# Performance work log

Hardware: AMD Instinct MI355X
Metric: run time of the kernel (lower is better)

## Reference

```python
import jax, jax.numpy as jnp
import numpy as np

B, T, C, H = 4, 1024, 512, 4
D = C // H
N_LAYER, LAYER_ID = 12, 1


def setup_inputs() -> dict:
    key = jax.random.key(0)
    ks = jax.random.split(key, 10)
    w = lambda k, shape: 0.02 * jax.random.normal(k, shape, dtype=jnp.float32)

    r01 = LAYER_ID / (N_LAYER - 1)          # ratio_0_to_1
    r1a0 = 1.0 - LAYER_ID / N_LAYER          # ratio_1_to_almost0
    i = np.arange(C, dtype=np.float32)
    time_decay = (-5.0 + 8.0 * (i / (C - 1)) ** (0.7 + 1.3 * r01)).astype(np.float32)
    xv = i / C
    tm_q = (xv ** r1a0).astype(np.float32)[None, None, :]
    tm_k = (xv ** r1a0).astype(np.float32)[None, None, :]
    tm_v = ((xv ** r1a0) + 0.3 * r01).astype(np.float32)[None, None, :]
    tm_g = (xv ** (0.5 * r1a0)).astype(np.float32)[None, None, :]

    return dict(
        x=jax.random.normal(ks[0], (B, T, C), dtype=jnp.float32),
        ln1_g=jnp.ones((C,), jnp.float32), ln1_b=jnp.zeros((C,), jnp.float32),
        ln2_g=jnp.ones((C,), jnp.float32), ln2_b=jnp.zeros((C,), jnp.float32),
        time_decay=jnp.asarray(time_decay),
        tm_q=jnp.asarray(tm_q), tm_k=jnp.asarray(tm_k),
        tm_v=jnp.asarray(tm_v), tm_g=jnp.asarray(tm_g),
        Wq=w(ks[1], (C, C)), Wk=w(ks[2], (C, C)), Wv=w(ks[3], (C, C)),
        Wg=w(ks[4], (C, C)), Wo=w(ks[5], (C, C)),
        rms_scale=jnp.ones((C,), jnp.float32),
        W1=w(ks[6], (4 * C, C)), W2=w(ks[7], (C, 4 * C)),
    )


def layernorm(x, g, b, eps=1e-5):
    m = x.mean(-1, keepdims=True)
    v = ((x - m) ** 2).mean(-1, keepdims=True)
    return g * (x - m) / jnp.sqrt(v + eps) + b


def rmsnorm(x, scale, eps=1e-8):
    # matches: norm = ||x||_2 / sqrt(dim); out = scale * x / (norm + eps)
    norm = jnp.sqrt(jnp.sum(x * x, axis=-1, keepdims=True)) / (x.shape[-1] ** 0.5)
    return scale * (x / (norm + eps))


def lnssm_scan(q, k, v, lam):
    """Decayed linear-attention scan. q,k,v: [B,T,H,D]; lam: [H,D] (decay over k index).
    Returns S: [B,T,H,D] = q_t^T A_t, Zs: [B,T,H] = q_t . z_t."""
    qT, kT, vT = (jnp.moveaxis(a, 1, 0) for a in (q, k, v))  # [T,B,H,D]
    Bq = q.shape[0]
    A0 = jnp.zeros((Bq, q.shape[2], q.shape[3], q.shape[3]), q.dtype)
    z0 = jnp.zeros((Bq, q.shape[2], q.shape[3]), q.dtype)

    def step(carry, inp):
        A, z = carry
        qt, kt, vt = inp
        A = lam[None, :, :, None] * A + kt[..., None] * vt[..., None, :]  # [B,H,Dk,Dv]
        z = lam[None] * z + kt                                            # [B,H,Dk]
        St = jnp.einsum('bhi,bhij->bhj', qt, A)
        Zt = jnp.einsum('bhi,bhi->bh', qt, z)
        return (A, z), (St, Zt)

    _, (S, Zs) = jax.lax.scan(step, (A0, z0), (qT, kT, vT))
    return jnp.moveaxis(S, 0, 1), jnp.moveaxis(Zs, 0, 1)


def reference(x, ln1_g, ln1_b, ln2_g, ln2_b, time_decay, tm_q, tm_k, tm_v, tm_g,
              Wq, Wk, Wv, Wg, Wo, rms_scale, W1, W2):
    Bx, Tx, Cx = x.shape
    Hh, Dd = H, Cx // H

    # --- TimeMix on ln1(x) ---
    h = layernorm(x, ln1_g, ln1_b)
    xx = jnp.concatenate([jnp.zeros_like(h[:, :1]), h[:, :-1]], axis=1)  # time shift
    xq = h * tm_q + xx * (1 - tm_q)
    xk = h * tm_k + xx * (1 - tm_k)
    xv_ = h * tm_v + xx * (1 - tm_v)
    xg = h * tm_g + xx * (1 - tm_g)
    q = xq @ Wq.T
    k = xk @ Wk.T
    v = xv_ @ Wv.T
    g = jax.nn.sigmoid(xg @ Wg.T)
    q = jnp.exp(rmsnorm(q, rms_scale))
    k = jnp.exp(rmsnorm(k, rms_scale))

    lam = jnp.exp(-jnp.exp(time_decay)).reshape(Hh, Dd)
    qh = q.reshape(Bx, Tx, Hh, Dd)
    kh = k.reshape(Bx, Tx, Hh, Dd)
    vh = v.reshape(Bx, Tx, Hh, Dd)
    S, Zs = lnssm_scan(qh, kh, vh, lam)
    att = (S / Zs[..., None]).reshape(Bx, Tx, Cx)
    att = (g * att) @ Wo.T
    x = x + att

    # --- ChannelMix on ln2(x) ---
    h2 = layernorm(x, ln2_g, ln2_b)
    x = x + jax.nn.gelu(h2 @ W1.T, approximate=False) @ W2.T
    return x
```

## Files before the change

### kernel.cpp

```cpp
#include <hip/hip_runtime.h>
#include <math.h>

#define Bb 4
#define Tt 1024
#define Cc 512
#define Hh 4
#define Dd 128
#define Mrows (Bb*Tt)
#define NC 32
#define CL 32
#define AUGSZ (Dd*(Dd+1))
#define AUGSTRIDE (16*AUGSZ)
#define AUGB_CB 18432

typedef unsigned short u16;
typedef __attribute__((ext_vector_type(8))) short bf16x8;
typedef __attribute__((ext_vector_type(4))) float f32x4;

__device__ __forceinline__ float readlane_f(float v, int lane) {
  return __uint_as_float(__builtin_amdgcn_readlane(__float_as_uint(v), lane));
}
__device__ __forceinline__ u16 f2bf(float f) {
  unsigned u = __float_as_uint(f);
  unsigned r = (u + 0x7fffu + ((u >> 16) & 1u)) >> 16;
  return (u16)r;
}
__device__ __forceinline__ unsigned pack2(float a, float b) {
  return (unsigned)f2bf(a) | ((unsigned)f2bf(b) << 16);
}

__global__ __launch_bounds__(256) void ln_kernel(const float* __restrict__ x,
    const float* __restrict__ g, const float* __restrict__ bta, float* __restrict__ out)
{
  int row = blockIdx.x, tid = threadIdx.x;
  const float* xr = x + (size_t)row * Cc;
  float v0 = xr[tid], v1 = xr[tid + 256];
  float s = v0 + v1, s2 = v0*v0 + v1*v1;
  #pragma unroll
  for (int off = 32; off > 0; off >>= 1) {
    s  += __shfl_down(s,  off, 64);
    s2 += __shfl_down(s2, off, 64);
  }
  __shared__ float rs[4], rq[4];
  int w = tid >> 6;
  if ((tid & 63) == 0) { rs[w] = s; rq[w] = s2; }
  __syncthreads();
  float S  = rs[0]+rs[1]+rs[2]+rs[3];
  float S2 = rq[0]+rq[1]+rq[2]+rq[3];
  float mean = S * (1.0f/Cc);
  float var  = S2 * (1.0f/Cc) - mean*mean;
  float inv = rsqrtf(var + 1e-5f);
  out[(size_t)row*Cc + tid]       = g[tid]     * (v0-mean)*inv + bta[tid];
  out[(size_t)row*Cc + tid + 256] = g[tid+256] * (v1-mean)*inv + bta[tid+256];
}

__global__ __launch_bounds__(256) void ln2b_kernel(const float* __restrict__ x,
    const float* __restrict__ p0, const float* __restrict__ p1,
    const float* __restrict__ g, const float* __restrict__ bta,
    float* __restrict__ x1, u16* __restrict__ out)
{
  int row = blockIdx.x, tid = threadIdx.x;
  size_t r0 = (size_t)row * Cc + tid, r1 = r0 + 256;
  float v0 = x[r0] + p0[r0] + p1[r0];
  float v1 = x[r1] + p0[r1] + p1[r1];
  x1[r0] = v0; x1[r1] = v1;
  float s = v0 + v1, s2 = v0*v0 + v1*v1;
  #pragma unroll
  for (int off = 32; off > 0; off >>= 1) {
    s  += __shfl_down(s,  off, 64);
    s2 += __shfl_down(s2, off, 64);
  }
  __shared__ float rs[4], rq[4];
  int w = tid >> 6;
  if ((tid & 63) == 0) { rs[w] = s; rq[w] = s2; }
  __syncthreads();
  float S  = rs[0]+rs[1]+rs[2]+rs[3];
  float S2 = rq[0]+rq[1]+rq[2]+rq[3];
  float mean = S * (1.0f/Cc);
  float var  = S2 * (1.0f/Cc) - mean*mean;
  float inv = rsqrtf(var + 1e-5f);
  int c0 = tid, c1 = tid + 256;
  float o0 = g[c0] * (v0-mean)*inv + bta[c0];
  float o1 = g[c1] * (v1-mean)*inv + bta[c1];
  out[((size_t)(c0 >> 3) * Mrows + row) * 8 + (c0 & 7)] = f2bf(o0);
  out[((size_t)(c1 >> 3) * Mrows + row) * 8 + (c1 & 7)] = f2bf(o1);
}

__device__ __forceinline__ void mix_one(const float* tm, int c0,
    float4 ha, float4 hb, float4 xa, float4 xb, u16* dst, size_t i8)
{
  float4 ta = *(const float4*)(tm + c0);
  float4 tb = *(const float4*)(tm + c0 + 4);
  uint4 o;
  o.x = pack2(ha.x*ta.x + xa.x*(1.f-ta.x), ha.y*ta.y + xa.y*(1.f-ta.y));
  o.y = pack2(ha.z*ta.z + xa.z*(1.f-ta.z), ha.w*ta.w + xa.w*(1.f-ta.w));
  o.z = pack2(hb.x*tb.x + xb.x*(1.f-tb.x), hb.y*tb.y + xb.y*(1.f-tb.y));
  o.w = pack2(hb.z*tb.z + xb.z*(1.f-tb.z), hb.w*tb.w + xb.w*(1.f-tb.w));
  *(uint4*)(dst + i8) = o;
}

__global__ __launch_bounds__(256) void mix_kernel(const float* __restrict__ h,
    const float* __restrict__ tmq, const float* __restrict__ tmk,
    const float* __restrict__ tmv, const float* __restrict__ tmg,
    u16* __restrict__ xqb, u16* __restrict__ xkb,
    u16* __restrict__ xvb, u16* __restrict__ xgb)
{
  int i = blockIdx.x * 256 + threadIdx.x;
  int m = i & 4095, c0 = (i >> 12) << 3;
  const float* hp = h + (size_t)m*Cc + c0;
  float4 ha = *(const float4*)hp, hb = *(const float4*)(hp + 4);
  float4 xa = make_float4(0,0,0,0), xb = make_float4(0,0,0,0);
  if (m & 1023) { xa = *(const float4*)(hp - Cc); xb = *(const float4*)(hp - Cc + 4); }
  size_t i8 = (size_t)i * 8;
  mix_one(tmq, c0, ha, hb, xa, xb, xqb, i8);
  mix_one(tmk, c0, ha, hb, xa, xb, xkb, i8);
  mix_one(tmv, c0, ha, hb, xa, xb, xvb, i8);
  mix_one(tmg, c0, ha, hb, xa, xb, xgb, i8);
}

__global__ __launch_bounds__(256) void wconv_all_kernel(
    const float* __restrict__ Wq, const float* __restrict__ Wk,
    const float* __restrict__ Wv, const float* __restrict__ Wg,
    const float* __restrict__ Wo, const float* __restrict__ W1,
    const float* __restrict__ W2, u16* __restrict__ out)
{
  int blk = blockIdx.x;
  const float* src; u16* dst; int K, nshift;
  if (blk < 640) {
    int wsel = blk >> 7;
    src = wsel==0?Wq:wsel==1?Wk:wsel==2?Wv:wsel==3?Wg:Wo;
    dst = out + (size_t)wsel*262144; K = 512; nshift = 9; blk &= 127;
  } else if (blk < 1152) {
    src = W1; dst = out + (size_t)5*262144; K = 512; nshift = 11; blk -= 640;
  } else {
    src = W2; dst = out + (size_t)5*262144 + 1048576; K = 2048; nshift = 9; blk -= 1152;
  }
  int i = blk*256 + threadIdx.x;
  int n = i & ((1 << nshift) - 1), kg = i >> nshift;
  const float* p = src + (size_t)n * K + kg * 8;
  float4 a = *(const float4*)p, b = *(const float4*)(p + 4);
  uint4 o;
  o.x = pack2(a.x, a.y); o.y = pack2(a.z, a.w);
  o.z = pack2(b.x, b.y); o.w = pack2(b.z, b.w);
  *(uint4*)(dst + (size_t)i * 8) = o;
}

template<int MR, int NR, int KR>
__device__ __forceinline__ void gemm_core(const u16* __restrict__ A,
    const u16* __restrict__ W, const float* __restrict__ res,
    float* __restrict__ outf, u16* __restrict__ outb, int act,
    int m0, int n0, u16* Asm, u16* Bsm)
{
  const int tid = threadIdx.x, w = tid >> 6, l = tid & 63;
  const int wr = w >> 1, wc = w & 1;
  f32x4 acc[4][4];
  #pragma unroll
  for (int i = 0; i < 4; ++i)
    #pragma unroll
    for (int j = 0; j < 4; ++j) acc[i][j] = (f32x4){0.f,0.f,0.f,0.f};
  const int kgl = l >> 4, rl = l & 15;
  const int q = w * 4;

  #define STAGE(KT, BUF) do {                                               \
    _Pragma("unroll")                                                       \
    for (int ii = 0; ii < 4; ++ii) {                                        \
      int qq = q + ii;                                                      \
      int isB = qq >> 3, idx = qq & 7, kg = idx >> 1, hf = idx & 1;         \
      const u16* src = isB                                                  \
        ? W + ((size_t)((KT)*4 + kg) * NR + n0 + hf*64 + l) * 8             \
        : A + ((size_t)((KT)*4 + kg) * MR + m0 + hf*64 + l) * 8;            \
      u16* dst = (isB ? Bsm : Asm) + (BUF)*4096 + (kg * 128 + hf * 64) * 8; \
      __builtin_amdgcn_global_load_lds(                                     \
          (const __attribute__((address_space(1))) void*)src,               \
          (__attribute__((address_space(3))) void*)dst, 16, 0, 0);          \
    }                                                                       \
  } while (0)

  constexpr int nk = KR >> 5;
  STAGE(0, 0); STAGE(1, 1);
  int cur = 0;
  for (int kt = 0; kt < nk; ++kt) {
    if (kt == nk - 1) asm volatile("s_waitcnt vmcnt(0)" ::: "memory");
    else              asm volatile("s_waitcnt vmcnt(4)" ::: "memory");
    __builtin_amdgcn_s_barrier();
    bf16x8 af[4], bfr[4];
    #pragma unroll
    for (int f = 0; f < 4; ++f)
      af[f] = *(const bf16x8*)&Asm[cur*4096 + (kgl*128 + wr*64 + f*16 + rl) * 8];
    #pragma unroll
    for (int f = 0; f < 4; ++f)
      bfr[f] = *(const bf16x8*)&Bsm[cur*4096 + (kgl*128 + wc*64 + f*16 + rl) * 8];
    if (kt + 2 < nk) {
      int nb = cur + 2; if (nb >= 3) nb -= 3;
      STAGE(kt + 2, nb);
    }
    __builtin_amdgcn_s_setprio(1);
    #pragma unroll
    for (int i = 0; i < 4; ++i)
      #pragma unroll
      for (int j = 0; j < 4; ++j)
        acc[i][j] = __builtin_amdgcn_mfma_f32_16x16x32_bf16(af[i], bfr[j], acc[i][j], 0, 0, 0);
    __builtin_amdgcn_s_setprio(0);
    if (++cur == 3) cur = 0;
  }
  #undef STAGE

  const int rbase = (l >> 4) * 4, cn = l & 15;
  #pragma unroll
  for (int i = 0; i < 4; ++i) {
    #pragma unroll
    for (int j = 0; j < 4; ++j) {
      #pragma unroll
      for (int r = 0; r < 4; ++r) {
        int m = m0 + wr*64 + i*16 + rbase + r;
        int n = n0 + wc*64 + j*16 + cn;
        float vv = acc[i][j][r];
        if (res) vv += res[(size_t)m * NR + n];
        if (act == 1) vv = 0.5f*vv*(1.f + erff(vv * 0.70710678118f));
        else if (act == 2) vv = 1.f/(1.f + expf(-vv));
        if (outb) outb[((size_t)(n >> 3) * MR + m) * 8 + (n & 7)] = f2bf(vv);
        else outf[(size_t)m * NR + n] = vv;
      }
    }
  }
}

__global__ __launch_bounds__(256) void gemm_qkvg(const u16* __restrict__ xall,
    const u16* __restrict__ Wall, float* __restrict__ outall)
{
  __shared__ __align__(16) u16 Asm[3*4096];
  __shared__ __align__(16) u16 Bsm[3*4096];
  int z = blockIdx.z;
  const size_t E = (size_t)Mrows * Cc;
  gemm_core<Mrows,512,512>(xall + z*E, Wall + (size_t)z*262144, nullptr,
            outall + z*E, nullptr, z == 3 ? 2 : 0,
            blockIdx.y * 128, blockIdx.x * 128, Asm, Bsm);
}

__global__ __launch_bounds__(256) void gemm_wo(const u16* __restrict__ A,
    const u16* __restrict__ W, float* __restrict__ pbuf)
{
  __shared__ __align__(16) u16 Asm[3*4096];
  __shared__ __align__(16) u16 Bsm[3*4096];
  int z = blockIdx.z;
  const size_t E = (size_t)Mrows * Cc;
  gemm_core<Mrows,512,256>(A + (size_t)z*32*Mrows*8, W + (size_t)z*32*512*8, nullptr,
            pbuf + z*E, nullptr, 0, blockIdx.y * 128, blockIdx.x * 128, Asm, Bsm);
}

__global__ __launch_bounds__(256) void gemm_w1(const u16* __restrict__ A,
    const u16* __restrict__ W, u16* __restrict__ outb)
{
  __shared__ __align__(16) u16 Asm[3*4096];
  __shared__ __align__(16) u16 Bsm[3*4096];
  gemm_core<Mrows,2048,512>(A, W, nullptr, nullptr, outb, 1,
            blockIdx.y * 128, blockIdx.x * 128, Asm, Bsm);
}

__global__ __launch_bounds__(256) void gemm_w2(const u16* __restrict__ A,
    const u16* __restrict__ W, float* __restrict__ pbuf)
{
  __shared__ __align__(16) u16 Asm[3*4096];
  __shared__ __align__(16) u16 Bsm[3*4096];
  int z = blockIdx.z;
  const size_t E = (size_t)Mrows * Cc;
  gemm_core<Mrows,512,512>(A + (size_t)z*64*Mrows*8, W + (size_t)z*64*512*8, nullptr,
            pbuf + z*E, nullptr, 0, blockIdx.y * 128, blockIdx.x * 128, Asm, Bsm);
}

__global__ __launch_bounds__(256) void reduce4_kernel(const float* __restrict__ x1,
    const float* __restrict__ p, float* __restrict__ out)
{
  const size_t E = (size_t)Mrows * Cc;
  size_t f = ((size_t)blockIdx.x * 256 + threadIdx.x) * 4;
  float4 a = *(const float4*)(x1 + f);
  float4 q0 = *(const float4*)(p + f);
  float4 q1 = *(const float4*)(p + E + f);
  float4 q2 = *(const float4*)(p + 2*E + f);
  float4 q3 = *(const float4*)(p + 3*E + f);
  float4 o;
  o.x = a.x + q0.x + q1.x + q2.x + q3.x;
  o.y = a.y + q0.y + q1.y + q2.y + q3.y;
  o.z = a.z + q0.z + q1.z + q2.z + q3.z;
  o.w = a.w + q0.w + q1.w + q2.w + q3.w;
  *(float4*)(out + f) = o;
}

__global__ __launch_bounds__(256) void rmsexp_kernel(float* __restrict__ qm,
    float* __restrict__ km, const float* __restrict__ scale)
{
  int row = blockIdx.x, tid = threadIdx.x;
  float* xr = (blockIdx.y ? km : qm) + (size_t)row * Cc;
  float v0 = xr[tid], v1 = xr[tid+256];
  float s2 = v0*v0 + v1*v1;
  #pragma unroll
  for (int off = 32; off > 0; off >>= 1) s2 += __shfl_down(s2, off, 64);
  __shared__ float rq[4];
  int w = tid >> 6;
  if ((tid & 63) == 0) rq[w] = s2;
  __syncthreads();
  float S2 = rq[0]+rq[1]+rq[2]+rq[3];
  float norm = sqrtf(S2) * 0.044194173824159216f;
  float r = 1.f / (norm + 1e-8f);
  xr[tid]     = expf(scale[tid]     * v0 * r);
  xr[tid+256] = expf(scale[tid+256] * v1 * r);
}

__global__ __launch_bounds__(256) void chunk_state_kernel(const float* __restrict__ k,
    const float* __restrict__ v, const float* __restrict__ td, float* __restrict__ Aug)
{
  __shared__ float k_lds[CL][Dd];
  __shared__ float v_lds[CL][Dd];
  int blk = blockIdx.x; int c = blk & (NC-1); int bh = blk >> 5;
  int b = bh >> 2, h = bh & 3;
  int tid = threadIdx.x;
  size_t base = ((size_t)b*Tt + (size_t)c*CL)*Cc + h*Dd;
  #pragma unroll
  for (int r = 0; r < 4; ++r) {
    int idx4 = r*256 + tid;
    int s = idx4 >> 5; int i4 = (idx4 & 31) << 2;
    *(float4*)&k_lds[s][i4] = *(const float4*)&k[base + (size_t)s*Cc + i4];
    *(float4*)&v_lds[s][i4] = *(const float4*)&v[base + (size_t)s*Cc + i4];
  }
  __syncthreads();
  int iq = tid >> 3; int i0 = iq << 2;
  int jg = tid & 7;  int j0 = jg << 4;
  float lam4[4], powv[4], zacc[4];
  #pragma unroll
  for (int ci=0; ci<4; ++ci) {
    lam4[ci] = expf(-expf(td[h*Dd + i0 + ci]));
    powv[ci] = 1.f; zacc[ci] = 0.f;
  }
  float acc[4][16];
  #pragma unroll
  for (int ci=0; ci<4; ++ci)
    #pragma unroll
    for (int jj=0; jj<16; ++jj) acc[ci][jj] = 0.f;

  for (int s = CL-1; s >= 0; --s) {
    float4 k4 = *(const float4*)&k_lds[s][i0];
    float kw0 = powv[0]*k4.x, kw1 = powv[1]*k4.y, kw2 = powv[2]*k4.z, kw3 = powv[3]*k4.w;
    zacc[0]+=kw0; zacc[1]+=kw1; zacc[2]+=kw2; zacc[3]+=kw3;
    #pragma unroll
    for (int q4 = 0; q4 < 4; ++q4) {
      float4 v4 = *(const float4*)&v_lds[s][j0 + q4*4];
      float vv[4] = {v4.x, v4.y, v4.z, v4.w};
      #pragma unroll
      for (int u=0; u<4; ++u) {
        acc[0][q4*4+u] += kw0*vv[u];
        acc[1][q4*4+u] += kw1*vv[u];
        acc[2][q4*4+u] += kw2*vv[u];
        acc[3][q4*4+u] += kw3*vv[u];
      }
    }
    powv[0]*=lam4[0]; powv[1]*=lam4[1]; powv[2]*=lam4[2]; powv[3]*=lam4[3];
  }
  float* aug = Aug + ((size_t)c*16 + bh)*AUGSZ;
  #pragma unroll
  for (int jj=0; jj<16; ++jj) {
    int j = j0 + jj;
    float4 wv = make_float4(acc[0][jj], acc[1][jj], acc[2][jj], acc[3][jj]);
    *(float4*)&aug[(size_t)j*Dd + i0] = wv;
  }
  if (jg == 0)
    *(float4*)&aug[(size_t)Dd*Dd + i0] = make_float4(zacc[0],zacc[1],zacc[2],zacc[3]);
}

__global__ __launch_bounds__(256) void combine_kernel(const float* __restrict__ Aug,
    const float* __restrict__ td, u16* __restrict__ Augb)
{
  int idx = blockIdx.x*256 + threadIdx.x;
  int bh = blockIdx.y; int h = bh & 3;
  int j = idx >> 7, i = idx & 127;
  size_t aoff = (size_t)(i >> 3) * 1152 + (size_t)j * 8 + (i & 7);
  if (j >= 129) {
    for (int c = 0; c < NC; ++c)
      Augb[((size_t)c*16 + bh)*AUGB_CB + aoff] = 0;
    return;
  }
  float lamL = expf(-expf(td[h*Dd + i]) * (float)CL);
  const float* p = Aug + (size_t)bh*AUGSZ + (size_t)j*Dd + i;
  float prev = 0.f;
  for (int c = 0; c < NC; ++c) {
    float val = p[(size_t)c*AUGSTRIDE];
    Augb[((size_t)c*16 + bh)*AUGB_CB + aoff] = f2bf(prev);
    prev = lamL*prev + val;
  }
}

__global__ __launch_bounds__(256, 2) void scan_mfma_kernel(
    const float* __restrict__ q, const float* __restrict__ k,
    const float* __restrict__ v, const float* __restrict__ td,
    const u16* __restrict__ Augb, const float* __restrict__ gmat,
    u16* __restrict__ out)
{
  __shared__ float k_lds[32*192];
  __shared__ u16  qfrag[32*128];
  __shared__ u16  vfrag[4*1152];
  __shared__ float P32[32*33];
  __shared__ u16  pfrag[32*32];
  __shared__ float lam_lds[128];
  __shared__ float zbuf[32];

  const int tid = threadIdx.x;
  const int blk = blockIdx.x; const int c = blk & 31, bh = blk >> 5;
  const int b = bh >> 2, h = bh & 3;
  const int w = tid >> 6, l = tid & 63;
  const int t = (w << 3) + (l >> 3);
  const int is = l & 7;

  if (tid < 128) lam_lds[tid] = expf(-expf(td[h*Dd + tid]));

  const size_t rowbase = ((size_t)(b*Tt + c*CL + t))*Cc + h*Dd + is*16;

  float qv[16];
  {
    #pragma unroll
    for (int c4 = 0; c4 < 4; ++c4) {
      float4 q4 = *(const float4*)(q + rowbase + c4*4);
      qv[c4*4+0]=q4.x; qv[c4*4+1]=q4.y; qv[c4*4+2]=q4.z; qv[c4*4+3]=q4.w;
    }
    float lt = (float)(t + 1);
    u16 qt[16];
    #pragma unroll
    for (int e = 0; e < 16; ++e) {
      float el2 = -expf(td[h*Dd + is*16 + e]) * 1.4426950408889634f;
      qt[e] = f2bf(qv[e] * exp2f(el2 * lt));
    }
    #pragma unroll
    for (int hf = 0; hf < 2; ++hf) {
      int k8 = is*2 + hf;
      uint4 pk;
      pk.x = (unsigned)qt[hf*8+0] | ((unsigned)qt[hf*8+1]<<16);
      pk.y = (unsigned)qt[hf*8+2] | ((unsigned)qt[hf*8+3]<<16);
      pk.z = (unsigned)qt[hf*8+4] | ((unsigned)qt[hf*8+5]<<16);
      pk.w = (unsigned)qt[hf*8+6] | ((unsigned)qt[hf*8+7]<<16);
      *(uint4*)&qfrag[t*128 + ((k8 ^ (t&7))<<3)] = pk;
    }
  }
  #pragma unroll
  for (int c4 = 0; c4 < 4; ++c4)
    *(float4*)&k_lds[t*192 + is*24 + c4*4] = *(const float4*)(k + rowbase + c4*4);
  #pragma unroll
  for (int c4 = 0; c4 < 4; ++c4) {
    float4 v4 = *(const float4*)(v + rowbase + c4*4);
    int j0 = is*16 + c4*4;
    vfrag[(t>>3)*1152 + (j0+0)*8 + (t&7)] = f2bf(v4.x);
    vfrag[(t>>3)*1152 + (j0+1)*8 + (t&7)] = f2bf(v4.y);
    vfrag[(t>>3)*1152 + (j0+2)*8 + (t&7)] = f2bf(v4.z);
    vfrag[(t>>3)*1152 + (j0+3)*8 + (t&7)] = f2bf(v4.w);
  }
  if (tid < 32) vfrag[(tid>>3)*1152 + 128*8 + (tid&7)] = 0x3F80;
  if (tid < 240) {
    #pragma unroll
    for (int u = 0; u < 2; ++u) {
      int e = tid*2 + u;
      int ig = e / 120, rem = e % 120;
      vfrag[ig*1152 + (129 + rem/8)*8 + (rem&7)] = 0;
    }
  }
  __syncthreads();

  {
    float lamr[16], wrun[16];
    #pragma unroll
    for (int e4 = 0; e4 < 4; ++e4) {
      float4 l4 = *(const float4*)&lam_lds[is*16 + e4*4];
      lamr[e4*4+0]=l4.x; lamr[e4*4+1]=l4.y; lamr[e4*4+2]=l4.z; lamr[e4*4+3]=l4.w;
    }
    #pragma unroll
    for (int e = 0; e < 16; ++e) wrun[e] = 1.f;
    const int smax = (w << 3) + 7;
    for (int s = smax; s >= 0; --s) {
      float dot = 0.f;
      #pragma unroll
      for (int c4 = 0; c4 < 4; ++c4) {
        float4 k4 = *(const float4*)&k_lds[s*192 + is*24 + c4*4];
        dot = fmaf(qv[c4*4+0], k4.x*wrun[c4*4+0], dot);
        dot = fmaf(qv[c4*4+1], k4.y*wrun[c4*4+1], dot);
        dot = fmaf(qv[c4*4+2], k4.z*wrun[c4*4+2], dot);
        dot = fmaf(qv[c4*4+3], k4.w*wrun[c4*4+3], dot);
      }
      dot += __shfl_xor(dot, 1);
      dot += __shfl_xor(dot, 2);
      dot += __shfl_xor(dot, 4);
      bool act = (s <= t);
      if (act && is == 0) P32[t*33 + s] = dot;
      if (act) {
        #pragma unroll
        for (int e = 0; e < 16; ++e) wrun[e] *= lamr[e];
      }
    }
  }
  __syncthreads();
  {
    int tt = tid >> 3, s0 = (tid & 7) * 4;
    #pragma unroll
    for (int ss = 0; ss < 4; ++ss) {
      int s = s0 + ss;
      float val = (s <= tt) ? P32[tt*33 + s] : 0.f;
      pfrag[tt*32 + (((s>>3) ^ (tt&3))<<3) + (s&7)] = f2bf(val);
    }
  }
  __syncthreads();

  const int tau = w >> 1;
  const int jt0 = (w & 1) ? 5 : 0;
  const int njt = (w & 1) ? 4 : 5;
  const int rl = l & 15, kg = l >> 4;
  const int trow = tau*16 + rl;
  const u16* augb_base = Augb + ((size_t)c*16 + bh)*AUGB_CB;

  bf16x8 aq[4];
  #pragma unroll
  for (int kk = 0; kk < 4; ++kk)
    aq[kk] = *(const bf16x8*)&qfrag[trow*128 + ((((kk<<2)+kg) ^ (trow&7))<<3)];
  bf16x8 ap = *(const bf16x8*)&pfrag[trow*32 + ((kg ^ (trow&3))<<3)];

  f32x4 acc[5];
  #pragma unroll
  for (int u = 0; u < 5; ++u) acc[u] = (f32x4){0.f,0.f,0.f,0.f};

  #pragma unroll
  for (int u = 0; u < 5; ++u) {
    if (u < njt) {
      int jt = jt0 + u;
      #pragma unroll
      for (int kk = 0; kk < 4; ++kk) {
        bf16x8 bfr = *(const bf16x8*)&augb_base[(size_t)(((kk<<2)+kg)*1152 + (jt*16 + rl)*8)];
        acc[u] = __builtin_amdgcn_mfma_f32_16x16x32_bf16(aq[kk], bfr, acc[u], 0, 0, 0);
      }
      bf16x8 bv = *(const bf16x8*)&vfrag[kg*1152 + (jt*16 + rl)*8];
      acc[u] = __builtin_amdgcn_mfma_f32_16x16x32_bf16(ap, bv, acc[u], 0, 0, 0);
    }
  }
  if ((w & 1) && rl == 0) {
    #pragma unroll
    for (int r = 0; r < 4; ++r) zbuf[tau*16 + kg*4 + r] = acc[3][r];
  }
  __syncthreads();

  const int nout = (w & 1) ? 3 : 5;
  #pragma unroll
  for (int u = 0; u < 5; ++u) {
    if (u < nout) {
      int jt = jt0 + u;
      int cc = h*Dd + jt*16 + rl;
      #pragma unroll
      for (int r = 0; r < 4; ++r) {
        int tr = tau*16 + kg*4 + r;
        int m = b*Tt + c*CL + tr;
        float zv = zbuf[tr];
        float gv = gmat[(size_t)m*Cc + cc];
        out[((size_t)(cc >> 3) * Mrows + m) * 8 + (cc & 7)] = f2bf(gv * acc[u][r] / zv);
      }
    }
  }
}

extern "C" void kernel_launch(void* const* d_in, const int* in_sizes, int n_in,
                              void* d_out, int out_size, void* d_ws, size_t ws_size,
                              hipStream_t stream) {
  const float* x    = (const float*)d_in[0];
  const float* ln1g = (const float*)d_in[1];
  const float* ln1b = (const float*)d_in[2];
  const float* ln2g = (const float*)d_in[3];
  const float* ln2b = (const float*)d_in[4];
  const float* td   = (const float*)d_in[5];
  const float* tmq  = (const float*)d_in[6];
  const float* tmk  = (const float*)d_in[7];
  const float* tmv  = (const float*)d_in[8];
  const float* tmg  = (const float*)d_in[9];
  const float* Wq   = (const float*)d_in[10];
  const float* Wk   = (const float*)d_in[11];
  const float* Wv   = (const float*)d_in[12];
  const float* Wg   = (const float*)d_in[13];
  const float* Wo   = (const float*)d_in[14];
  const float* rsc  = (const float*)d_in[15];
  const float* W1   = (const float*)d_in[16];
  const float* W2   = (const float*)d_in[17];
  float* ws = (float*)d_ws;
  const size_t E = (size_t)Mrows*Cc;
  float* s0 = ws;
  float* s1 = ws + E;
  float* s2 = ws + 2*E;
  float* s3 = ws + 3*E;
  float* x1 = ws + 4*E;
  u16* xqb = (u16*)(ws + 5*E);
  u16* xkb = xqb + E;
  u16* xvb = xkb + E;
  u16* xgb = xvb + E;
  float* Aug = ws + 7*E;
  u16* midb = (u16*)Aug;
  float* wreg = ws + 7*E + (size_t)NC*16*AUGSZ;
  u16* Wqb = (u16*)wreg;
  u16* W1b = Wqb + 5*262144;
  u16* W2b = W1b + 1048576;
  u16* Wob = Wqb + 4*262144;
  u16* Augb = W2b + 1048576;
  u16* gattb = xqb;
  u16* h2b   = xkb;

  wconv_all_kernel<<<1664,256,0,stream>>>(Wq, Wk, Wv, Wg, Wo, W1, W2, Wqb);

  ln_kernel<<<Mrows,256,0,stream>>>(x, ln1g, ln1b, s0);
  mix_kernel<<<1024,256,0,stream>>>(s0, tmq,tmk,tmv,tmg, xqb,xkb,xvb,xgb);
  gemm_qkvg<<<dim3(4,32,4),256,0,stream>>>(xqb, Wqb, s0);
  rmsexp_kernel<<<dim3(Mrows,2),256,0,stream>>>(s0, s1, rsc);
  chunk_state_kernel<<<16*NC,256,0,stream>>>(s1, s2, td, Aug);
  combine_kernel<<<dim3(72,16),256,0,stream>>>(Aug, td, Augb);
  scan_mfma_kernel<<<16*NC,256,0,stream>>>(s0, s1, s2, td, Augb, s3, gattb);
  gemm_wo<<<dim3(4,32,2),256,0,stream>>>(gattb, Wob, s2);
  ln2b_kernel<<<Mrows,256,0,stream>>>(x, s2, s3, ln2g, ln2b, x1, h2b);
  gemm_w1<<<dim3(16,32),256,0,stream>>>(h2b, W1b, midb);
  gemm_w2<<<dim3(4,32,4),256,0,stream>>>(midb, W2b, s0);
  reduce4_kernel<<<2048,256,0,stream>>>(x1, s0, (float*)d_out);
}
```

Baseline: 168.3 us.

## Fuse LN1 with time-mix, fold RMS-exp into GEMM epilogue and scan kernels

Merges layernorm and token-shift mixing into one kernel that recomputes the previous row's layernorm instead of round-tripping through a float buffer. Removes the separate rmsexp pass: the QKVG GEMM epilogue writes per-row partial sums of squares, and chunk_state and scan apply the normalisation and exp on load. Chunk states are stored in bf16 in the fragment layout, which shrinks combine traffic and drops the zero-padding writes. In exchange, q/k exps are computed redundantly in two kernels, the GEMM epilogue gains extra syncs, and the bf16 intermediate state costs precision.

```diff
diff --git a/kernel.cpp b/kernel.cpp
--- a/kernel.cpp
+++ b/kernel.cpp
@@ -9,49 +9,73 @@
 #define Mrows (Bb*Tt)
 #define NC 32
 #define CL 32
-#define AUGSZ (Dd*(Dd+1))
-#define AUGSTRIDE (16*AUGSZ)
 #define AUGB_CB 18432
 
 typedef unsigned short u16;
 typedef __attribute__((ext_vector_type(8))) short bf16x8;
 typedef __attribute__((ext_vector_type(4))) float f32x4;
 
-__device__ __forceinline__ float readlane_f(float v, int lane) {
-  return __uint_as_float(__builtin_amdgcn_readlane(__float_as_uint(v), lane));
-}
 __device__ __forceinline__ u16 f2bf(float f) {
   unsigned u = __float_as_uint(f);
   unsigned r = (u + 0x7fffu + ((u >> 16) & 1u)) >> 16;
   return (u16)r;
 }
+__device__ __forceinline__ float bf2f(u16 v) {
+  return __uint_as_float((unsigned)v << 16);
+}
 __device__ __forceinline__ unsigned pack2(float a, float b) {
   return (unsigned)f2bf(a) | ((unsigned)f2bf(b) << 16);
 }
-
-__global__ __launch_bounds__(256) void ln_kernel(const float* __restrict__ x,
-    const float* __restrict__ g, const float* __restrict__ bta, float* __restrict__ out)
-{
-  int row = blockIdx.x, tid = threadIdx.x;
-  const float* xr = x + (size_t)row * Cc;
+__device__ __forceinline__ float rms_r(const float* __restrict__ ssqp, int zsel, int row) {
+  const float* p = ssqp + (size_t)zsel*4*Mrows + row;
+  float s2 = p[0] + p[Mrows] + p[2*Mrows] + p[3*Mrows];
+  float norm = sqrtf(s2) * 0.044194173824159216f;
+  return 1.f / (norm + 1e-8f);
+}
+
+__global__ __launch_bounds__(256) void ln1mix_kernel(const float* __restrict__ x,
+    const float* __restrict__ g, const float* __restrict__ bta,
+    const float* __restrict__ tmq, const float* __restrict__ tmk,
+    const float* __restrict__ tmv, const float* __restrict__ tmg,
+    u16* __restrict__ xqb, u16* __restrict__ xkb,
+    u16* __restrict__ xvb, u16* __restrict__ xgb)
+{
+  int m = blockIdx.x, tid = threadIdx.x;
+  const float* xr = x + (size_t)m * Cc;
   float v0 = xr[tid], v1 = xr[tid + 256];
-  float s = v0 + v1, s2 = v0*v0 + v1*v1;
+  bool has = (m & (Tt-1)) != 0;
+  float u0 = 0.f, u1 = 0.f;
+  if (has) { u0 = xr[tid - Cc]; u1 = xr[(int)tid + 256 - Cc]; }
+  float sa = v0 + v1, qa = v0*v0 + v1*v1;
+  float sb = u0 + u1, qb = u0*u0 + u1*u1;
   #pragma unroll
   for (int off = 32; off > 0; off >>= 1) {
-    s  += __shfl_down(s,  off, 64);
-    s2 += __shfl_down(s2, off, 64);
-  }
-  __shared__ float rs[4], rq[4];
+    sa += __shfl_down(sa, off, 64); qa += __shfl_down(qa, off, 64);
+    sb += __shfl_down(sb, off, 64); qb += __shfl_down(qb, off, 64);
+  }
+  __shared__ float r4[4][4];
   int w = tid >> 6;
-  if ((tid & 63) == 0) { rs[w] = s; rq[w] = s2; }
+  if ((tid & 63) == 0) { r4[w][0]=sa; r4[w][1]=qa; r4[w][2]=sb; r4[w][3]=qb; }
   __syncthreads();
-  float S  = rs[0]+rs[1]+rs[2]+rs[3];
-  float S2 = rq[0]+rq[1]+rq[2]+rq[3];
-  float mean = S * (1.0f/Cc);
-  float var  = S2 * (1.0f/Cc) - mean*mean;
-  float inv = rsqrtf(var + 1e-5f);
-  out[(size_t)row*Cc + tid]       = g[tid]     * (v0-mean)*inv + bta[tid];
-  out[(size_t)row*Cc + tid + 256] = g[tid+256] * (v1-mean)*inv + bta[tid+256];
+  float Sa = r4[0][0]+r4[1][0]+r4[2][0]+r4[3][0];
+  float Qa = r4[0][1]+r4[1][1]+r4[2][1]+r4[3][1];
+  float Sb = r4[0][2]+r4[1][2]+r4[2][2]+r4[3][2];
+  float Qb = r4[0][3]+r4[1][3]+r4[2][3]+r4[3][3];
+  float ma = Sa*(1.f/Cc), va = Qa*(1.f/Cc) - ma*ma, ia = rsqrtf(va + 1e-5f);
+  float mb = Sb*(1.f/Cc), vb = Qb*(1.f/Cc) - mb*mb, ib = rsqrtf(vb + 1e-5f);
+  #pragma unroll
+  for (int half = 0; half < 2; ++half) {
+    int c = tid + half*256;
+    float v = half ? v1 : v0, u = half ? u1 : u0;
+    float hv = g[c]*(v - ma)*ia + bta[c];
+    float pv = has ? (g[c]*(u - mb)*ib + bta[c]) : 0.f;
+    size_t off = ((size_t)(c >> 3) * Mrows + m) * 8 + (c & 7);
+    float tq = tmq[c], tk = tmk[c], tv = tmv[c], tg = tmg[c];
+    xqb[off] = f2bf(hv*tq + pv*(1.f-tq));
+    xkb[off] = f2bf(hv*tk + pv*(1.f-tk));
+    xvb[off] = f2bf(hv*tv + pv*(1.f-tv));
+    xgb[off] = f2bf(hv*tg + pv*(1.f-tg));
+  }
 }
 
 __global__ __launch_bounds__(256) void ln2b_kernel(const float* __restrict__ x,
@@ -86,38 +110,6 @@
   out[((size_t)(c1 >> 3) * Mrows + row) * 8 + (c1 & 7)] = f2bf(o1);
 }
 
-__device__ __forceinline__ void mix_one(const float* tm, int c0,
-    float4 ha, float4 hb, float4 xa, float4 xb, u16* dst, size_t i8)
-{
-  float4 ta = *(const float4*)(tm + c0);
-  float4 tb = *(const float4*)(tm + c0 + 4);
-  uint4 o;
-  o.x = pack2(ha.x*ta.x + xa.x*(1.f-ta.x), ha.y*ta.y + xa.y*(1.f-ta.y));
-  o.y = pack2(ha.z*ta.z + xa.z*(1.f-ta.z), ha.w*ta.w + xa.w*(1.f-ta.w));
-  o.z = pack2(hb.x*tb.x + xb.x*(1.f-tb.x), hb.y*tb.y + xb.y*(1.f-tb.y));
-  o.w = pack2(hb.z*tb.z + xb.z*(1.f-tb.z), hb.w*tb.w + xb.w*(1.f-tb.w));
-  *(uint4*)(dst + i8) = o;
-}
-
-__global__ __launch_bounds__(256) void mix_kernel(const float* __restrict__ h,
-    const float* __restrict__ tmq, const float* __restrict__ tmk,
-    const float* __restrict__ tmv, const float* __restrict__ tmg,
-    u16* __restrict__ xqb, u16* __restrict__ xkb,
-    u16* __restrict__ xvb, u16* __restrict__ xgb)
-{
-  int i = blockIdx.x * 256 + threadIdx.x;
-  int m = i & 4095, c0 = (i >> 12) << 3;
-  const float* hp = h + (size_t)m*Cc + c0;
-  float4 ha = *(const float4*)hp, hb = *(const float4*)(hp + 4);
-  float4 xa = make_float4(0,0,0,0), xb = make_float4(0,0,0,0);
-  if (m & 1023) { xa = *(const float4*)(hp - Cc); xb = *(const float4*)(hp - Cc + 4); }
-  size_t i8 = (size_t)i * 8;
-  mix_one(tmq, c0, ha, hb, xa, xb, xqb, i8);
-  mix_one(tmk, c0, ha, hb, xa, xb, xkb, i8);
-  mix_one(tmv, c0, ha, hb, xa, xb, xvb, i8);
-  mix_one(tmg, c0, ha, hb, xa, xb, xgb, i8);
-}
-
 __global__ __launch_bounds__(256) void wconv_all_kernel(
     const float* __restrict__ Wq, const float* __restrict__ Wk,
     const float* __restrict__ Wv, const float* __restrict__ Wg,
@@ -149,7 +141,7 @@
 __device__ __forceinline__ void gemm_core(const u16* __restrict__ A,
     const u16* __restrict__ W, const float* __restrict__ res,
     float* __restrict__ outf, u16* __restrict__ outb, int act,
-    int m0, int n0, u16* Asm, u16* Bsm)
+    int m0, int n0, u16* Asm, u16* Bsm, float* __restrict__ ssq)
 {
   const int tid = threadIdx.x, w = tid >> 6, l = tid & 63;
   const int wr = w >> 1, wc = w & 1;
@@ -223,18 +215,42 @@
       }
     }
   }
+
+  if (ssq) {
+    __syncthreads();
+    float* red2 = (float*)Asm;
+    #pragma unroll
+    for (int i = 0; i < 4; ++i) {
+      #pragma unroll
+      for (int r = 0; r < 4; ++r) {
+        int row_local = wr*64 + i*16 + rbase + r;
+        float sq = 0.f;
+        #pragma unroll
+        for (int j = 0; j < 4; ++j) { float t = acc[i][j][r]; sq += t*t; }
+        red2[row_local*32 + wc*16 + cn] = sq;
+      }
+    }
+    __syncthreads();
+    if (tid < 128) {
+      float ssum = 0.f;
+      #pragma unroll
+      for (int u2 = 0; u2 < 32; ++u2) ssum += red2[tid*32 + u2];
+      ssq[m0 + tid] = ssum;
+    }
+  }
 }
 
 __global__ __launch_bounds__(256) void gemm_qkvg(const u16* __restrict__ xall,
-    const u16* __restrict__ Wall, float* __restrict__ outall)
+    const u16* __restrict__ Wall, float* __restrict__ outall, float* __restrict__ ssqp)
 {
   __shared__ __align__(16) u16 Asm[3*4096];
   __shared__ __align__(16) u16 Bsm[3*4096];
   int z = blockIdx.z;
   const size_t E = (size_t)Mrows * Cc;
+  float* ssq = (z < 2) ? ssqp + ((size_t)z*4 + blockIdx.x)*Mrows : nullptr;
   gemm_core<Mrows,512,512>(xall + z*E, Wall + (size_t)z*262144, nullptr,
             outall + z*E, nullptr, z == 3 ? 2 : 0,
-            blockIdx.y * 128, blockIdx.x * 128, Asm, Bsm);
+            blockIdx.y * 128, blockIdx.x * 128, Asm, Bsm, ssq);
 }
 
 __global__ __launch_bounds__(256) void gemm_wo(const u16* __restrict__ A,
@@ -245,7 +261,7 @@
   int z = blockIdx.z;
   const size_t E = (size_t)Mrows * Cc;
   gemm_core<Mrows,512,256>(A + (size_t)z*32*Mrows*8, W + (size_t)z*32*512*8, nullptr,
-            pbuf + z*E, nullptr, 0, blockIdx.y * 128, blockIdx.x * 128, Asm, Bsm);
+            pbuf + z*E, nullptr, 0, blockIdx.y * 128, blockIdx.x * 128, Asm, Bsm, nullptr);
 }
 
 __global__ __launch_bounds__(256) void gemm_w1(const u16* __restrict__ A,
@@ -254,7 +270,7 @@
   __shared__ __align__(16) u16 Asm[3*4096];
   __shared__ __align__(16) u16 Bsm[3*4096];
   gemm_core<Mrows,2048,512>(A, W, nullptr, nullptr, outb, 1,
-            blockIdx.y * 128, blockIdx.x * 128, Asm, Bsm);
+            blockIdx.y * 128, blockIdx.x * 128, Asm, Bsm, nullptr);
 }
 
 __global__ __launch_bounds__(256) void gemm_w2(const u16* __restrict__ A,
@@ -265,7 +281,7 @@
   int z = blockIdx.z;
   const size_t E = (size_t)Mrows * Cc;
   gemm_core<Mrows,512,512>(A + (size_t)z*64*Mrows*8, W + (size_t)z*64*512*8, nullptr,
-            pbuf + z*E, nullptr, 0, blockIdx.y * 128, blockIdx.x * 128, Asm, Bsm);
+            pbuf + z*E, nullptr, 0, blockIdx.y * 128, blockIdx.x * 128, Asm, Bsm, nullptr);
 }
 
 __global__ __launch_bounds__(256) void reduce4_kernel(const float* __restrict__ x1,
@@ -286,28 +302,10 @@
   *(float4*)(out + f) = o;
 }
 
-__global__ __launch_bounds__(256) void rmsexp_kernel(float* __restrict__ qm,
-    float* __restrict__ km, const float* __restrict__ scale)
-{
-  int row = blockIdx.x, tid = threadIdx.x;
-  float* xr = (blockIdx.y ? km : qm) + (size_t)row * Cc;
-  float v0 = xr[tid], v1 = xr[tid+256];
-  float s2 = v0*v0 + v1*v1;
-  #pragma unroll
-  for (int off = 32; off > 0; off >>= 1) s2 += __shfl_down(s2, off, 64);
-  __shared__ float rq[4];
-  int w = tid >> 6;
-  if ((tid & 63) == 0) rq[w] = s2;
-  __syncthreads();
-  float S2 = rq[0]+rq[1]+rq[2]+rq[3];
-  float norm = sqrtf(S2) * 0.044194173824159216f;
-  float r = 1.f / (norm + 1e-8f);
-  xr[tid]     = expf(scale[tid]     * v0 * r);
-  xr[tid+256] = expf(scale[tid+256] * v1 * r);
-}
-
 __global__ __launch_bounds__(256) void chunk_state_kernel(const float* __restrict__ k,
-    const float* __restrict__ v, const float* __restrict__ td, float* __restrict__ Aug)
+    const float* __restrict__ v, const float* __restrict__ td,
+    const float* __restrict__ rsc, const float* __restrict__ ssqp,
+    u16* __restrict__ Augl)
 {
   __shared__ float k_lds[CL][Dd];
   __shared__ float v_lds[CL][Dd];
@@ -319,7 +317,12 @@
   for (int r = 0; r < 4; ++r) {
     int idx4 = r*256 + tid;
     int s = idx4 >> 5; int i4 = (idx4 & 31) << 2;
-    *(float4*)&k_lds[s][i4] = *(const float4*)&k[base + (size_t)s*Cc + i4];
+    float rk = rms_r(ssqp, 1, b*Tt + c*CL + s);
+    float4 kr = *(const float4*)&k[base + (size_t)s*Cc + i4];
+    k_lds[s][i4+0] = expf(rsc[h*Dd+i4+0] * kr.x * rk);
+    k_lds[s][i4+1] = expf(rsc[h*Dd+i4+1] * kr.y * rk);
+    k_lds[s][i4+2] = expf(rsc[h*Dd+i4+2] * kr.z * rk);
+    k_lds[s][i4+3] = expf(rsc[h*Dd+i4+3] * kr.w * rk);
     *(float4*)&v_lds[s][i4] = *(const float4*)&v[base + (size_t)s*Cc + i4];
   }
   __syncthreads();
@@ -355,35 +358,40 @@
     }
     powv[0]*=lam4[0]; powv[1]*=lam4[1]; powv[2]*=lam4[2]; powv[3]*=lam4[3];
   }
-  float* aug = Aug + ((size_t)c*16 + bh)*AUGSZ;
+  u16* aug = Augl + ((size_t)c*16 + bh)*AUGB_CB;
+  const int ig = i0 >> 3, isub = i0 & 7;
   #pragma unroll
   for (int jj=0; jj<16; ++jj) {
     int j = j0 + jj;
-    float4 wv = make_float4(acc[0][jj], acc[1][jj], acc[2][jj], acc[3][jj]);
-    *(float4*)&aug[(size_t)j*Dd + i0] = wv;
-  }
-  if (jg == 0)
-    *(float4*)&aug[(size_t)Dd*Dd + i0] = make_float4(zacc[0],zacc[1],zacc[2],zacc[3]);
-}
-
-__global__ __launch_bounds__(256) void combine_kernel(const float* __restrict__ Aug,
+    uint2 pk;
+    pk.x = pack2(acc[0][jj], acc[1][jj]);
+    pk.y = pack2(acc[2][jj], acc[3][jj]);
+    *(uint2*)&aug[(size_t)ig*1152 + (size_t)j*8 + isub] = pk;
+  }
+  if (jg == 0) {
+    uint2 pk;
+    pk.x = pack2(zacc[0], zacc[1]);
+    pk.y = pack2(zacc[2], zacc[3]);
+    *(uint2*)&aug[(size_t)ig*1152 + 128*8 + isub] = pk;
+  }
+}
+
+__global__ __launch_bounds__(256) void combine_kernel(const u16* __restrict__ Augl,
     const float* __restrict__ td, u16* __restrict__ Augb)
 {
   int idx = blockIdx.x*256 + threadIdx.x;
+  if (idx >= 129*128) return;
   int bh = blockIdx.y; int h = bh & 3;
   int j = idx >> 7, i = idx & 127;
   size_t aoff = (size_t)(i >> 3) * 1152 + (size_t)j * 8 + (i & 7);
-  if (j >= 129) {
-    for (int c = 0; c < NC; ++c)
-      Augb[((size_t)c*16 + bh)*AUGB_CB + aoff] = 0;
-    return;
-  }
   float lamL = expf(-expf(td[h*Dd + i]) * (float)CL);
-  const float* p = Aug + (size_t)bh*AUGSZ + (size_t)j*Dd + i;
+  const u16* pl = Augl + (size_t)bh*AUGB_CB + aoff;
+  u16* pi = Augb + (size_t)bh*AUGB_CB + aoff;
   float prev = 0.f;
+  const size_t cstr = (size_t)16*AUGB_CB;
   for (int c = 0; c < NC; ++c) {
-    float val = p[(size_t)c*AUGSTRIDE];
-    Augb[((size_t)c*16 + bh)*AUGB_CB + aoff] = f2bf(prev);
+    float val = bf2f(pl[c*cstr]);
+    pi[c*cstr] = f2bf(prev);
     prev = lamL*prev + val;
   }
 }
@@ -391,6 +399,7 @@
 __global__ __launch_bounds__(256, 2) void scan_mfma_kernel(
     const float* __restrict__ q, const float* __restrict__ k,
     const float* __restrict__ v, const float* __restrict__ td,
+    const float* __restrict__ rsc, const float* __restrict__ ssqp,
     const u16* __restrict__ Augb, const float* __restrict__ gmat,
     u16* __restrict__ out)
 {
@@ -411,14 +420,21 @@
 
   if (tid < 128) lam_lds[tid] = expf(-expf(td[h*Dd + tid]));
 
-  const size_t rowbase = ((size_t)(b*Tt + c*CL + t))*Cc + h*Dd + is*16;
+  const int grow = b*Tt + c*CL + t;
+  const size_t rowbase = ((size_t)grow)*Cc + h*Dd + is*16;
+  const float rq = rms_r(ssqp, 0, grow);
+  const float rk = rms_r(ssqp, 1, grow);
 
   float qv[16];
   {
     #pragma unroll
     for (int c4 = 0; c4 < 4; ++c4) {
       float4 q4 = *(const float4*)(q + rowbase + c4*4);
-      qv[c4*4+0]=q4.x; qv[c4*4+1]=q4.y; qv[c4*4+2]=q4.z; qv[c4*4+3]=q4.w;
+      int e0 = c4*4;
+      qv[e0+0] = expf(rsc[h*Dd+is*16+e0+0] * q4.x * rq);
+      qv[e0+1] = expf(rsc[h*Dd+is*16+e0+1] * q4.y * rq);
+      qv[e0+2] = expf(rsc[h*Dd+is*16+e0+2] * q4.z * rq);
+      qv[e0+3] = expf(rsc[h*Dd+is*16+e0+3] * q4.w * rq);
     }
     float lt = (float)(t + 1);
     u16 qt[16];
@@ -439,8 +455,14 @@
     }
   }
   #pragma unroll
-  for (int c4 = 0; c4 < 4; ++c4)
-    *(float4*)&k_lds[t*192 + is*24 + c4*4] = *(const float4*)(k + rowbase + c4*4);
+  for (int c4 = 0; c4 < 4; ++c4) {
+    float4 k4 = *(const float4*)(k + rowbase + c4*4);
+    int e0 = is*16 + c4*4;
+    k_lds[t*192 + is*24 + c4*4+0] = expf(rsc[h*Dd+e0+0] * k4.x * rk);
+    k_lds[t*192 + is*24 + c4*4+1] = expf(rsc[h*Dd+e0+1] * k4.y * rk);
+    k_lds[t*192 + is*24 + c4*4+2] = expf(rsc[h*Dd+e0+2] * k4.z * rk);
+    k_lds[t*192 + is*24 + c4*4+3] = expf(rsc[h*Dd+e0+3] * k4.w * rk);
+  }
   #pragma unroll
   for (int c4 = 0; c4 < 4; ++c4) {
     float4 v4 = *(const float4*)(v + rowbase + c4*4);
@@ -590,26 +612,25 @@
   u16* xkb = xqb + E;
   u16* xvb = xkb + E;
   u16* xgb = xvb + E;
-  float* Aug = ws + 7*E;
-  u16* midb = (u16*)Aug;
-  float* wreg = ws + 7*E + (size_t)NC*16*AUGSZ;
-  u16* Wqb = (u16*)wreg;
-  u16* W1b = Wqb + 5*262144;
+  u16* wreg = (u16*)(ws + 7*E);
+  u16* Wqb = wreg;
+  u16* Wob = wreg + 4*262144;
+  u16* W1b = wreg + 5*262144;
   u16* W2b = W1b + 1048576;
-  u16* Wob = Wqb + 4*262144;
-  u16* Augb = W2b + 1048576;
+  u16* Augl = W2b + 1048576;
+  u16* Augb = Augl + (size_t)NC*16*AUGB_CB;
+  float* ssqp = (float*)(Augb + (size_t)NC*16*AUGB_CB);
+  u16* midb  = Augl;
   u16* gattb = xqb;
   u16* h2b   = xkb;
 
   wconv_all_kernel<<<1664,256,0,stream>>>(Wq, Wk, Wv, Wg, Wo, W1, W2, Wqb);
-
-  ln_kernel<<<Mrows,256,0,stream>>>(x, ln1g, ln1b, s0);
-  mix_kernel<<<1024,256,0,stream>>>(s0, tmq,tmk,tmv,tmg, xqb,xkb,xvb,xgb);
-  gemm_qkvg<<<dim3(4,32,4),256,0,stream>>>(xqb, Wqb, s0);
-  rmsexp_kernel<<<dim3(Mrows,2),256,0,stream>>>(s0, s1, rsc);
-  chunk_state_kernel<<<16*NC,256,0,stream>>>(s1, s2, td, Aug);
-  combine_kernel<<<dim3(72,16),256,0,stream>>>(Aug, td, Augb);
-  scan_mfma_kernel<<<16*NC,256,0,stream>>>(s0, s1, s2, td, Augb, s3, gattb);
+  ln1mix_kernel<<<Mrows,256,0,stream>>>(x, ln1g, ln1b, tmq,tmk,tmv,tmg,
+                                        xqb,xkb,xvb,xgb);
+  gemm_qkvg<<<dim3(4,32,4),256,0,stream>>>(xqb, Wqb, s0, ssqp);
+  chunk_state_kernel<<<16*NC,256,0,stream>>>(s1, s2, td, rsc, ssqp, Augl);
+  combine_kernel<<<dim3(65,16),256,0,stream>>>(Augl, td, Augb);
+  scan_mfma_kernel<<<16*NC,256,0,stream>>>(s0, s1, s2, td, rsc, ssqp, Augb, s3, gattb);
   gemm_wo<<<dim3(4,32,2),256,0,stream>>>(gattb, Wob, s2);
   ln2b_kernel<<<Mrows,256,0,stream>>>(x, s2, s3, ln2g, ln2b, x1, h2b);
   gemm_w1<<<dim3(16,32),256,0,stream>>>(h2b, W1b, midb);
```

New measurement: 168.9 us. About the same (+0.4%).
